# Kernel tuning notes

Measured on AMD Instinct MI355X. Metric: run time of the kernel, lower is better.

Reference implementation:

```python
import jax, jax.numpy as jnp
import numpy as np

HEADS = 8
DIM_HEAD = 32  # dim // heads


def setup_inputs() -> dict:
    key = jax.random.key(0)
    ks = jax.random.split(key, 5)
    B, C, H, W = 4, 256, 48, 48
    return {
        "x": jax.random.normal(ks[0], (B, C, H, W), jnp.float32),
        "Wqkv": jax.random.normal(ks[1], (3 * C, C), jnp.float32) * (C ** -0.5),
        "bqkv": jax.random.normal(ks[2], (3 * C,), jnp.float32) * 0.02,
        "W0": jax.random.normal(ks[3], (C, C), jnp.float32) * (C ** -0.5),
        "b0": jax.random.normal(ks[4], (C,), jnp.float32) * 0.02,
    }


def reference(x, Wqkv, bqkv, W0, b0):
    b, c, h, w = x.shape
    m, d = HEADS, DIM_HEAD
    n = h * w
    scale = d ** -0.5
    # 1x1 conv == per-pixel GEMM: [b,3c,h,w]
    qkv = jnp.einsum('bchw,oc->bohw', x, Wqkv) + bqkv[None, :, None, None]
    # rearrange 'b (d k m) h w -> k b m (h w) d' (channel factors as d, then k, then m)
    qkv = qkv.reshape(b, d, 3, m, n)            # [b, d, 3, m, n]
    qkv = jnp.transpose(qkv, (2, 0, 3, 4, 1))   # [3, b, m, n, d]
    q, k, v = qkv[0], qkv[1], qkv[2]
    scores = jnp.einsum('bmid,bmjd->bmij', q, k) * scale  # [b, m, n, n]
    attn = jax.nn.softmax(scores, axis=-1)
    out = jnp.einsum('bmij,bmjd->bmid', attn, v)          # [b, m, n, d]
    # rearrange 'b m (h w) d -> b (m d) h w'
    out = jnp.transpose(out, (0, 1, 3, 2)).reshape(b, m * d, h, w)
    out = jnp.einsum('bchw,oc->bohw', out, W0) + b0[None, :, None, None]
    return out
```

## Files before the change

kernel.cpp:

```cpp
#include <hip/hip_runtime.h>
#include <hip/hip_bf16.h>

#define NPIX 2304
#define C_IN 256
#define NHEADS 8
#define DHEAD 32

typedef float f32x4 __attribute__((ext_vector_type(4)));
typedef __bf16 bf16x8 __attribute__((ext_vector_type(8)));
typedef __bf16 bf16x4 __attribute__((ext_vector_type(4)));

#if __has_builtin(__builtin_amdgcn_exp2f)
#define EXP2F(x) __builtin_amdgcn_exp2f(x)
#else
#define EXP2F(x) exp2f(x)
#endif

__device__ inline void gload_lds16(const void* g, void* l) {
    __builtin_amdgcn_global_load_lds(
        (const __attribute__((address_space(1))) unsigned int*)g,
        (__attribute__((address_space(3))) unsigned int*)l, 16, 0, 0);
}

__global__ __launch_bounds__(256) void prep_w(
    const float* __restrict__ Wq, const float* __restrict__ W0,
    __bf16* __restrict__ wq, __bf16* __restrict__ w0)
{
    const int r = blockIdx.x;
    const int c = threadIdx.x;
    float v;
    __bf16* dst;
    if (r < 768) { v = Wq[r * 256 + c];         dst = wq + (size_t)r * 512; }
    else         { v = W0[(r - 768) * 256 + c]; dst = w0 + (size_t)(r - 768) * 512; }
    __bf16 hb = (__bf16)v;
    dst[c]       = hb;
    dst[256 + c] = (__bf16)(v - (float)hb);
}

__global__ __launch_bounds__(256) void prep_x(
    const float* __restrict__ x, __bf16* __restrict__ xt)
{
    __shared__ unsigned int lds[64 * 69];
    const int t  = threadIdx.x;
    const int n0 = blockIdx.x * 64;
    const int c0 = blockIdx.y * 64;
    const int b  = blockIdx.z;
    const float* xb = x + (size_t)b * C_IN * NPIX;

    #pragma unroll
    for (int p = 0; p < 4; ++p) {
        const int r    = (t >> 4) + p * 16;
        const int ncol = (t & 15) * 4;
        float4 v = *(const float4*)&xb[(size_t)(c0 + r) * NPIX + n0 + ncol];
        float a[4] = {v.x, v.y, v.z, v.w};
        #pragma unroll
        for (int i = 0; i < 4; ++i)
            lds[r * 69 + ncol + i] =
                (unsigned int)__builtin_bit_cast(unsigned short, (__bf16)a[i]);
    }
    __syncthreads();

    #pragma unroll
    for (int p = 0; p < 2; ++p) {
        const int nn = (t >> 3) + p * 32;
        const int ch = t & 7;
        bf16x8 h8;
        #pragma unroll
        for (int i = 0; i < 8; ++i)
            h8[i] = __builtin_bit_cast(__bf16,
                        (unsigned short)lds[(ch * 8 + i) * 69 + nn]);
        *(bf16x8*)&xt[((size_t)b * NPIX + n0 + nn) * 256 + c0 + ch * 8] = h8;
    }
}

__global__ __launch_bounds__(256) void qkv_mfma(
    const __bf16* __restrict__ wq, const __bf16* __restrict__ xt,
    const float* __restrict__ bias, float* __restrict__ qg,
    __bf16* __restrict__ khi, __bf16* __restrict__ vg)
{
    __shared__ alignas(16) unsigned char sm[32768];
    const int tid = threadIdx.x;
    const int l   = tid & 63;
    const int w   = tid >> 6;
    const int g   = l >> 4;
    const int c16 = l & 15;

    const int id  = blockIdx.x;
    const int xcd = id & 7;
    const int li  = id >> 3;
    const int pnl = xcd * 9 + li / 6;
    const int mt  = li % 6;
    const int b   = pnl / 18;
    const int nt  = pnl - b * 18;
    const int n0  = nt * 128;
    const int p0  = mt * 128;
    const int kq  = mt >> 1;

    const int wr = (w >> 1) * 64;
    const int wc = (w & 1) * 64;
    f32x4 acc[4][4] = {};

#define STG(buf, ks)                                                           \
    {                                                                          \
        unsigned char* lbs = sm + (buf) * 16384;                               \
        _Pragma("unroll")                                                      \
        for (int i = 0; i < 2; ++i) {                                          \
            const int row = i * 64 + (tid >> 2);                               \
            const int cl  = tid & 3;                                           \
            const int cg  = cl ^ (row & 3);                                    \
            const int pA  = p0 + row;                                          \
            const int oA  = 24 * ((pA & 255) >> 3) + 8 * kq + (pA & 7);        \
            gload_lds16(wq + (size_t)oA * 512 + (ks) * 32 + cg * 8,            \
                        lbs + row * 64 + cl * 16);                             \
            gload_lds16(xt + ((size_t)b * NPIX + n0 + row) * 256 +             \
                            ((ks) & 7) * 32 + cg * 8,                          \
                        lbs + 8192 + row * 64 + cl * 16);                      \
        }                                                                      \
    }

    STG(0, 0);
    __syncthreads();
    for (int ks = 0; ks < 16; ++ks) {
        const int buf = ks & 1;
        if (ks + 1 < 16) STG(buf ^ 1, ks + 1);
        unsigned char* lb = sm + buf * 16384;
        bf16x8 af[4], bff[4];
        #pragma unroll
        for (int oi = 0; oi < 4; ++oi) {
            const int ra = wr + oi * 16 + c16;
            af[oi] = *(bf16x8*)(lb + ra * 64 + ((g ^ (ra & 3)) * 16));
        }
        #pragma unroll
        for (int ni = 0; ni < 4; ++ni) {
            const int rb = wc + ni * 16 + c16;
            bff[ni] = *(bf16x8*)(lb + 8192 + rb * 64 + ((g ^ (rb & 3)) * 16));
        }
        #pragma unroll
        for (int oi = 0; oi < 4; ++oi)
            #pragma unroll
            for (int ni = 0; ni < 4; ++ni)
                acc[oi][ni] = __builtin_amdgcn_mfma_f32_16x16x32_bf16(
                    af[oi], bff[ni], acc[oi][ni], 0, 0, 0);
        __syncthreads();
    }
#undef STG

    const float qscale = 0.17677669529663687f * 1.4426950408889634f;
    #pragma unroll
    for (int oi = 0; oi < 4; ++oi) {
        #pragma unroll
        for (int rr = 0; rr < 4; ++rr) {
            const int p = p0 + wr + oi * 16 + 4 * g + rr;
            const int d = (p & 255) >> 3;
            const int h = p & 7;
            const int o = 24 * d + 8 * kq + h;
            const float bi = bias[o];
            const int bh_ = b * NHEADS + h;
            #pragma unroll
            for (int ni = 0; ni < 4; ++ni) {
                const int n = n0 + wc + ni * 16 + c16;
                const float val = acc[oi][ni][rr] + bi;
                if (kq == 0) {
                    qg[((size_t)bh_ * DHEAD + d) * NPIX + n] = val * qscale;
                } else if (kq == 1) {
                    const int cp = ((d >> 3) + (n >> 1)) & 3;
                    khi[((size_t)bh_ * NPIX + n) * 32 + cp * 8 + (d & 7)] = (__bf16)val;
                } else {
                    const int cp = ((n >> 3) & 7) ^ (d & 7);
                    vg[((size_t)bh_ * DHEAD + d) * NPIX + (n >> 6) * 64 + cp * 8 + (n & 7)]
                        = (__bf16)val;
                }
            }
        }
    }
}

__global__ __launch_bounds__(256) void attn_mfma(
    const float* __restrict__ qg, const __bf16* __restrict__ khi,
    const __bf16* __restrict__ vg,
    float* __restrict__ po, float* __restrict__ lw)
{
    __shared__ alignas(16) unsigned char sm[32768];
    const int tid = threadIdx.x;
    const int l   = tid & 63;
    const int w   = tid >> 6;
    const int g   = l >> 4;
    const int c16 = l & 15;

    const int id = blockIdx.x;
    const int lg = (id & 7) * 144 + (id >> 3);
    const int bh = lg / 36;
    const int rem = lg - bh * 36;
    const int half = rem / 18;
    const int qt = rem - half * 18;

    const float*  qb  = qg  + (size_t)bh * DHEAD * NPIX;
    const __bf16* khb = khi + (size_t)bh * NPIX * 32;
    const __bf16* vb  = vg  + (size_t)bh * DHEAD * NPIX;

    const int q0 = qt * 128 + w * 32;

    bf16x8 qh[2], ql[2];
    #pragma unroll
    for (int qgi = 0; qgi < 2; ++qgi)
        #pragma unroll
        for (int e = 0; e < 8; ++e) {
            float v = qb[(size_t)(g * 8 + e) * NPIX + q0 + qgi * 16 + c16];
            __bf16 hb = (__bf16)v;
            qh[qgi][e] = hb;
            ql[qgi][e] = (__bf16)(v - (float)hb);
        }

    f32x4 o[2][2] = {};
    float lsum[2] = {0.f, 0.f};

    const int vd   = w * 8 + (l >> 3);
    const int kswz = (c16 >> 1) & 3;
    unsigned char* const wsl = sm + 16384 + w * 4096;

#define STAGE(buf, kb)                                                         \
    {                                                                          \
        const int j0s = (kb) * 64;                                             \
        unsigned char* lbs = sm + (buf) * 8192;                                \
        gload_lds16(khb + (size_t)(j0s + w * 16) * 32 + l * 8, lbs + w * 1024);\
        gload_lds16(vb + (size_t)vd * NPIX + j0s + (l & 7) * 8,                \
                    lbs + 4096 + w * 1024);                                    \
    }

    const int kb0 = half * 18;
    STAGE(0, kb0);
    __syncthreads();

    for (int t = 0; t < 18; ++t) {
        const int buf = t & 1;
        if (t + 1 < 18) STAGE(buf ^ 1, kb0 + t + 1);
        unsigned char* lb = sm + buf * 8192;

        f32x4 sv[2][4];
        __builtin_amdgcn_s_setprio(1);
        #pragma unroll
        for (int f = 0; f < 4; ++f) {
            const int ko = (c16 + 16 * f) * 64 + ((g + kswz) & 3) * 16;
            bf16x8 kh8 = *(bf16x8*)(lb + ko);
            #pragma unroll
            for (int qgi = 0; qgi < 2; ++qgi) {
                f32x4 acc = {0.f, 0.f, 0.f, 0.f};
                acc = __builtin_amdgcn_mfma_f32_16x16x32_bf16(kh8, ql[qgi], acc, 0, 0, 0);
                acc = __builtin_amdgcn_mfma_f32_16x16x32_bf16(kh8, qh[qgi], acc, 0, 0, 0);
                sv[qgi][f] = acc;
            }
        }
        __builtin_amdgcn_s_setprio(0);

        #pragma unroll
        for (int qgi = 0; qgi < 2; ++qgi) {
            float rs = 0.f;
            __bf16 pb[16];
            #pragma unroll
            for (int f = 0; f < 4; ++f)
                #pragma unroll
                for (int rr = 0; rr < 4; ++rr) {
                    const float p = EXP2F(sv[qgi][f][rr]);
                    rs += p;
                    pb[f * 4 + rr] = (__bf16)p;
                }
            lsum[qgi] += rs;
            const int qrow = qgi * 16 + c16;
            #pragma unroll
            for (int f = 0; f < 4; ++f) {
                const int ch = (2 * f + (g >> 1)) ^ (c16 & 7);
                *(bf16x4*)(wsl + qrow * 128 + ch * 16 + (g & 1) * 8) =
                    *(bf16x4*)&pb[f * 4];
            }
        }

        __builtin_amdgcn_s_setprio(1);
        #pragma unroll
        for (int kc = 0; kc < 2; ++kc) {
            const int vch = (((g + 4 * kc) ^ (c16 & 7))) * 16;
            bf16x8 va0 = *(bf16x8*)(lb + 4096 + c16 * 128 + vch);
            bf16x8 va1 = *(bf16x8*)(lb + 4096 + (16 + c16) * 128 + vch);
            #pragma unroll
            for (int qgi = 0; qgi < 2; ++qgi) {
                bf16x8 pf = *(bf16x8*)(wsl + (qgi * 16 + c16) * 128 + vch);
                o[qgi][0] = __builtin_amdgcn_mfma_f32_16x16x32_bf16(va0, pf, o[qgi][0], 0, 0, 0);
                o[qgi][1] = __builtin_amdgcn_mfma_f32_16x16x32_bf16(va1, pf, o[qgi][1], 0, 0, 0);
            }
        }
        __builtin_amdgcn_s_setprio(0);

        __syncthreads();
    }
#undef STAGE

    #pragma unroll
    for (int qgi = 0; qgi < 2; ++qgi) {
        lsum[qgi] += __shfl_xor(lsum[qgi], 16);
        lsum[qgi] += __shfl_xor(lsum[qgi], 32);
        const int n = q0 + qgi * 16 + c16;
        const size_t rbase = ((size_t)(half * 32 + bh) * NPIX + n) * 32;
        #pragma unroll
        for (int dh = 0; dh < 2; ++dh)
            *(f32x4*)&po[rbase + dh * 16 + 4 * g] = o[qgi][dh];
        if (g == 0)
            lw[(size_t)(half * 32 + bh) * NPIX + n] = lsum[qgi];
    }
}

__global__ __launch_bounds__(256) void combine(
    const float* __restrict__ po, const float* __restrict__ lw,
    __bf16* __restrict__ aw)
{
    const int t  = threadIdx.x;
    const int nn = t >> 6;
    const int r  = t & 63;
    const int h  = r >> 3;
    const int d4 = (r & 7) * 4;
    const int n0 = blockIdx.x * 16;
    const int b  = blockIdx.y;
    const int bh = b * NHEADS + h;

    #pragma unroll
    for (int p = 0; p < 4; ++p) {
        const int n = n0 + p * 4 + nn;
        const float inv = 1.0f / (lw[(size_t)bh * NPIX + n] +
                                  lw[(size_t)(32 + bh) * NPIX + n]);
        f32x4 O0 = *(const f32x4*)&po[((size_t)bh * NPIX + n) * 32 + d4];
        f32x4 O1 = *(const f32x4*)&po[((size_t)(32 + bh) * NPIX + n) * 32 + d4];
        bf16x4 hv;
        #pragma unroll
        for (int i = 0; i < 4; ++i)
            hv[i] = (__bf16)((O0[i] + O1[i]) * inv);
        *(bf16x4*)&aw[((size_t)b * NPIX + n) * 256 + h * 32 + d4] = hv;
    }
}

__global__ __launch_bounds__(256) void out_mfma(
    const __bf16* __restrict__ w0, const __bf16* __restrict__ aw,
    const float* __restrict__ bias, float* __restrict__ out)
{
    __shared__ alignas(16) unsigned char sm[32768];
    const int tid = threadIdx.x;
    const int l   = tid & 63;
    const int w   = tid >> 6;
    const int g   = l >> 4;
    const int c16 = l & 15;

    const int id  = blockIdx.x;
    const int xcd = id & 7;
    const int li  = id >> 3;
    const int pnl = xcd * 9 + (li >> 1);
    const int mt  = li & 1;
    const int b   = pnl / 18;
    const int nt  = pnl - b * 18;
    const int n0  = nt * 128;
    const int o0  = mt * 128;

    const int wr = (w >> 1) * 64;
    const int wc = (w & 1) * 64;
    f32x4 acc[4][4] = {};

#define STG(buf, ks)                                                           \
    {                                                                          \
        unsigned char* lbs = sm + (buf) * 16384;                               \
        _Pragma("unroll")                                                      \
        for (int i = 0; i < 2; ++i) {                                          \
            const int row = i * 64 + (tid >> 2);                               \
            const int cl  = tid & 3;                                           \
            const int cg  = cl ^ (row & 3);                                    \
            gload_lds16(w0 + (size_t)(o0 + row) * 512 + (ks) * 32 + cg * 8,    \
                        lbs + row * 64 + cl * 16);                             \
            gload_lds16(aw + ((size_t)b * NPIX + n0 + row) * 256 +             \
                            ((ks) & 7) * 32 + cg * 8,                          \
                        lbs + 8192 + row * 64 + cl * 16);                      \
        }                                                                      \
    }

    STG(0, 0);
    __syncthreads();
    for (int ks = 0; ks < 16; ++ks) {
        const int buf = ks & 1;
        if (ks + 1 < 16) STG(buf ^ 1, ks + 1);
        unsigned char* lb = sm + buf * 16384;
        bf16x8 af[4], bff[4];
        #pragma unroll
        for (int oi = 0; oi < 4; ++oi) {
            const int ra = wr + oi * 16 + c16;
            af[oi] = *(bf16x8*)(lb + ra * 64 + ((g ^ (ra & 3)) * 16));
        }
        #pragma unroll
        for (int ni = 0; ni < 4; ++ni) {
            const int rb = wc + ni * 16 + c16;
            bff[ni] = *(bf16x8*)(lb + 8192 + rb * 64 + ((g ^ (rb & 3)) * 16));
        }
        #pragma unroll
        for (int oi = 0; oi < 4; ++oi)
            #pragma unroll
            for (int ni = 0; ni < 4; ++ni)
                acc[oi][ni] = __builtin_amdgcn_mfma_f32_16x16x32_bf16(
                    af[oi], bff[ni], acc[oi][ni], 0, 0, 0);
        __syncthreads();
    }
#undef STG

    #pragma unroll
    for (int oi = 0; oi < 4; ++oi) {
        #pragma unroll
        for (int rr = 0; rr < 4; ++rr) {
            const int o = o0 + wr + oi * 16 + 4 * g + rr;
            const float bi = bias[o];
            #pragma unroll
            for (int ni = 0; ni < 4; ++ni) {
                const int n = n0 + wc + ni * 16 + c16;
                out[((size_t)b * C_IN + o) * NPIX + n] = acc[oi][ni][rr] + bi;
            }
        }
    }
}

extern "C" void kernel_launch(void* const* d_in, const int* in_sizes, int n_in,
                              void* d_out, int out_size, void* d_ws, size_t ws_size,
                              hipStream_t stream) {
    const float* x    = (const float*)d_in[0];
    const float* Wqkv = (const float*)d_in[1];
    const float* bqkv = (const float*)d_in[2];
    const float* W0   = (const float*)d_in[3];
    const float* b0   = (const float*)d_in[4];
    float* out = (float*)d_out;

    char* ws = (char*)d_ws;
    __bf16* wq  = (__bf16*)(ws);
    __bf16* w0  = (__bf16*)(ws + 786432);
    __bf16* xt  = (__bf16*)(ws + 1048576);
    float*  qg  = (float*) (ws + 5767168);
    __bf16* khi = (__bf16*)(ws + 15204352);
    __bf16* vg  = (__bf16*)(ws + 19922944);
    float*  po  = (float*) (ws + 24641536);
    float*  lw  = (float*) (ws + 43515904);
    __bf16* aw  = xt;

    prep_w<<<1024, 256, 0, stream>>>(Wqkv, W0, wq, w0);
    prep_x<<<dim3(NPIX / 64, C_IN / 64, 4), 256, 0, stream>>>(x, xt);
    qkv_mfma<<<dim3(432), 256, 0, stream>>>(wq, xt, bqkv, qg, khi, vg);
    attn_mfma<<<dim3(1152), 256, 0, stream>>>(qg, khi, vg, po, lw);
    combine<<<dim3(NPIX / 16, 4), 256, 0, stream>>>(po, lw, aw);
    out_mfma<<<dim3(144), 256, 0, stream>>>(w0, aw, b0, out);
}
```

Baseline: 159.2 us.

## Fuse prep kernels, fold combine into output GEMM, restructure split-bf16 K loop

Measured after the change: 156.8 us. Within noise of the previous version (-1.5%).

```diff
diff --git a/kernel.cpp b/kernel.cpp
--- a/kernel.cpp
+++ b/kernel.cpp
@@ -22,29 +22,31 @@
         (__attribute__((address_space(3))) unsigned int*)l, 16, 0, 0);
 }
 
-__global__ __launch_bounds__(256) void prep_w(
+__global__ __launch_bounds__(256) void prep_wx(
     const float* __restrict__ Wq, const float* __restrict__ W0,
-    __bf16* __restrict__ wq, __bf16* __restrict__ w0)
-{
-    const int r = blockIdx.x;
-    const int c = threadIdx.x;
-    float v;
-    __bf16* dst;
-    if (r < 768) { v = Wq[r * 256 + c];         dst = wq + (size_t)r * 512; }
-    else         { v = W0[(r - 768) * 256 + c]; dst = w0 + (size_t)(r - 768) * 512; }
-    __bf16 hb = (__bf16)v;
-    dst[c]       = hb;
-    dst[256 + c] = (__bf16)(v - (float)hb);
-}
-
-__global__ __launch_bounds__(256) void prep_x(
-    const float* __restrict__ x, __bf16* __restrict__ xt)
+    const float* __restrict__ x,
+    __bf16* __restrict__ wq, __bf16* __restrict__ w0,
+    __bf16* __restrict__ xt)
 {
     __shared__ unsigned int lds[64 * 69];
+    const int id = blockIdx.x;
     const int t  = threadIdx.x;
-    const int n0 = blockIdx.x * 64;
-    const int c0 = blockIdx.y * 64;
-    const int b  = blockIdx.z;
+
+    if (id >= 576) {
+        const int r = id - 576;
+        float v;
+        __bf16* dst;
+        if (r < 768) { v = Wq[r * 256 + t];         dst = wq + (size_t)r * 512; }
+        else         { v = W0[(r - 768) * 256 + t]; dst = w0 + (size_t)(r - 768) * 512; }
+        __bf16 hb = (__bf16)v;
+        dst[t]       = hb;
+        dst[256 + t] = (__bf16)(v - (float)hb);
+        return;
+    }
+
+    const int n0 = (id % 36) * 64;
+    const int c0 = ((id / 36) & 3) * 64;
+    const int b  = id / 144;
     const float* xb = x + (size_t)b * C_IN * NPIX;
 
     #pragma unroll
@@ -78,7 +80,7 @@
     const float* __restrict__ bias, float* __restrict__ qg,
     __bf16* __restrict__ khi, __bf16* __restrict__ vg)
 {
-    __shared__ alignas(16) unsigned char sm[32768];
+    __shared__ alignas(16) unsigned char sm[49152];
     const int tid = threadIdx.x;
     const int l   = tid & 63;
     const int w   = tid >> 6;
@@ -100,47 +102,59 @@
     const int wc = (w & 1) * 64;
     f32x4 acc[4][4] = {};
 
-#define STG(buf, ks)                                                           \
+#define STG(buf, cs)                                                           \
     {                                                                          \
-        unsigned char* lbs = sm + (buf) * 16384;                               \
+        unsigned char* lbs = sm + (buf) * 24576;                               \
+        _Pragma("unroll")                                                      \
+        for (int i = 0; i < 4; ++i) {                                          \
+            const int row = i * 64 + (tid >> 2);                               \
+            const int cl  = tid & 3;                                           \
+            const int cg  = cl ^ (row & 3);                                    \
+            const int pr  = p0 + (row & 127);                                  \
+            const int oA  = 24 * ((pr & 255) >> 3) + 8 * kq + (pr & 7);        \
+            gload_lds16(wq + (size_t)oA * 512 + (i >> 1) * 256 +               \
+                            (cs) * 32 + cg * 8,                                \
+                        lbs + row * 64 + cl * 16);                             \
+        }                                                                      \
         _Pragma("unroll")                                                      \
         for (int i = 0; i < 2; ++i) {                                          \
             const int row = i * 64 + (tid >> 2);                               \
             const int cl  = tid & 3;                                           \
             const int cg  = cl ^ (row & 3);                                    \
-            const int pA  = p0 + row;                                          \
-            const int oA  = 24 * ((pA & 255) >> 3) + 8 * kq + (pA & 7);        \
-            gload_lds16(wq + (size_t)oA * 512 + (ks) * 32 + cg * 8,            \
-                        lbs + row * 64 + cl * 16);                             \
             gload_lds16(xt + ((size_t)b * NPIX + n0 + row) * 256 +             \
-                            ((ks) & 7) * 32 + cg * 8,                          \
-                        lbs + 8192 + row * 64 + cl * 16);                      \
+                            (cs) * 32 + cg * 8,                                \
+                        lbs + 16384 + row * 64 + cl * 16);                     \
         }                                                                      \
     }
 
     STG(0, 0);
     __syncthreads();
-    for (int ks = 0; ks < 16; ++ks) {
-        const int buf = ks & 1;
-        if (ks + 1 < 16) STG(buf ^ 1, ks + 1);
-        unsigned char* lb = sm + buf * 16384;
-        bf16x8 af[4], bff[4];
+    #pragma unroll
+    for (int cs = 0; cs < 8; ++cs) {
+        const int buf = cs & 1;
+        if (cs + 1 < 8) STG(buf ^ 1, cs + 1);
+        unsigned char* lb = sm + buf * 24576;
+        bf16x8 ah[4], al4[4], bf4[4];
         #pragma unroll
         for (int oi = 0; oi < 4; ++oi) {
             const int ra = wr + oi * 16 + c16;
-            af[oi] = *(bf16x8*)(lb + ra * 64 + ((g ^ (ra & 3)) * 16));
+            ah[oi]  = *(bf16x8*)(lb + ra * 64 + ((g ^ (ra & 3)) * 16));
+            al4[oi] = *(bf16x8*)(lb + (128 + ra) * 64 + ((g ^ (ra & 3)) * 16));
         }
         #pragma unroll
         for (int ni = 0; ni < 4; ++ni) {
             const int rb = wc + ni * 16 + c16;
-            bff[ni] = *(bf16x8*)(lb + 8192 + rb * 64 + ((g ^ (rb & 3)) * 16));
+            bf4[ni] = *(bf16x8*)(lb + 16384 + rb * 64 + ((g ^ (rb & 3)) * 16));
         }
         #pragma unroll
         for (int oi = 0; oi < 4; ++oi)
             #pragma unroll
-            for (int ni = 0; ni < 4; ++ni)
+            for (int ni = 0; ni < 4; ++ni) {
                 acc[oi][ni] = __builtin_amdgcn_mfma_f32_16x16x32_bf16(
-                    af[oi], bff[ni], acc[oi][ni], 0, 0, 0);
+                    ah[oi], bf4[ni], acc[oi][ni], 0, 0, 0);
+                acc[oi][ni] = __builtin_amdgcn_mfma_f32_16x16x32_bf16(
+                    al4[oi], bf4[ni], acc[oi][ni], 0, 0, 0);
+            }
         __syncthreads();
     }
 #undef STG
@@ -307,39 +321,12 @@
     }
 }
 
-__global__ __launch_bounds__(256) void combine(
-    const float* __restrict__ po, const float* __restrict__ lw,
-    __bf16* __restrict__ aw)
+__global__ __launch_bounds__(256) void out_mfma(
+    const __bf16* __restrict__ w0, const float* __restrict__ po,
+    const float* __restrict__ lw, const float* __restrict__ bias,
+    float* __restrict__ out)
 {
-    const int t  = threadIdx.x;
-    const int nn = t >> 6;
-    const int r  = t & 63;
-    const int h  = r >> 3;
-    const int d4 = (r & 7) * 4;
-    const int n0 = blockIdx.x * 16;
-    const int b  = blockIdx.y;
-    const int bh = b * NHEADS + h;
-
-    #pragma unroll
-    for (int p = 0; p < 4; ++p) {
-        const int n = n0 + p * 4 + nn;
-        const float inv = 1.0f / (lw[(size_t)bh * NPIX + n] +
-                                  lw[(size_t)(32 + bh) * NPIX + n]);
-        f32x4 O0 = *(const f32x4*)&po[((size_t)bh * NPIX + n) * 32 + d4];
-        f32x4 O1 = *(const f32x4*)&po[((size_t)(32 + bh) * NPIX + n) * 32 + d4];
-        bf16x4 hv;
-        #pragma unroll
-        for (int i = 0; i < 4; ++i)
-            hv[i] = (__bf16)((O0[i] + O1[i]) * inv);
-        *(bf16x4*)&aw[((size_t)b * NPIX + n) * 256 + h * 32 + d4] = hv;
-    }
-}
-
-__global__ __launch_bounds__(256) void out_mfma(
-    const __bf16* __restrict__ w0, const __bf16* __restrict__ aw,
-    const float* __restrict__ bias, float* __restrict__ out)
-{
-    __shared__ alignas(16) unsigned char sm[32768];
+    __shared__ alignas(16) unsigned char sm[51200];
     const int tid = threadIdx.x;
     const int l   = tid & 63;
     const int w   = tid >> 6;
@@ -360,48 +347,97 @@
     const int wc = (w & 1) * 64;
     f32x4 acc[4][4] = {};
 
-#define STG(buf, ks)                                                           \
+    const int brow = tid >> 1;
+    const int bch  = tid & 1;
+
+#define STG_A(buf, cs)                                                         \
     {                                                                          \
-        unsigned char* lbs = sm + (buf) * 16384;                               \
+        unsigned char* lbs = sm + (buf) * 25600;                               \
         _Pragma("unroll")                                                      \
-        for (int i = 0; i < 2; ++i) {                                          \
+        for (int i = 0; i < 4; ++i) {                                          \
             const int row = i * 64 + (tid >> 2);                               \
             const int cl  = tid & 3;                                           \
             const int cg  = cl ^ (row & 3);                                    \
-            gload_lds16(w0 + (size_t)(o0 + row) * 512 + (ks) * 32 + cg * 8,    \
+            gload_lds16(w0 + (size_t)(o0 + (row & 127)) * 512 +                \
+                            (i >> 1) * 256 + (cs) * 32 + cg * 8,               \
                         lbs + row * 64 + cl * 16);                             \
-            gload_lds16(aw + ((size_t)b * NPIX + n0 + row) * 256 +             \
-                            ((ks) & 7) * 32 + cg * 8,                          \
-                        lbs + 8192 + row * 64 + cl * 16);                      \
         }                                                                      \
     }
 
-    STG(0, 0);
+    f32x4 r0[4], r1[4];
+    float il;
+
+#define LDB(cs)                                                                \
+    {                                                                          \
+        const int bh_ = b * 8 + (cs);                                          \
+        const int n   = n0 + brow;                                             \
+        const float l0 = lw[(size_t)bh_ * NPIX + n];                           \
+        const float l1 = lw[(size_t)(32 + bh_) * NPIX + n];                    \
+        il = 1.0f / (l0 + l1);                                                 \
+        const float* s0 = &po[((size_t)bh_ * NPIX + n) * 32 + bch * 16];       \
+        const float* s1 = &po[((size_t)(32 + bh_) * NPIX + n) * 32 + bch * 16];\
+        _Pragma("unroll")                                                      \
+        for (int k2 = 0; k2 < 4; ++k2) {                                       \
+            r0[k2] = *(const f32x4*)(s0 + k2 * 4);                             \
+            r1[k2] = *(const f32x4*)(s1 + k2 * 4);                             \
+        }                                                                      \
+    }
+
+#define WRB(buf)                                                               \
+    {                                                                          \
+        unsigned char* lbs = sm + (buf) * 25600 + 16384;                       \
+        _Pragma("unroll")                                                      \
+        for (int k2 = 0; k2 < 2; ++k2) {                                       \
+            bf16x8 v8;                                                         \
+            _Pragma("unroll")                                                  \
+            for (int e = 0; e < 4; ++e) {                                      \
+                v8[e]     = (__bf16)((r0[2 * k2][e]     + r1[2 * k2][e])     * il); \
+                v8[4 + e] = (__bf16)((r0[2 * k2 + 1][e] + r1[2 * k2 + 1][e]) * il); \
+            }                                                                  \
+            *(bf16x8*)(lbs + brow * 72 + bch * 32 + k2 * 16) = v8;             \
+        }                                                                      \
+    }
+
+    STG_A(0, 0);
+    LDB(0);
+    WRB(0);
     __syncthreads();
-    for (int ks = 0; ks < 16; ++ks) {
-        const int buf = ks & 1;
-        if (ks + 1 < 16) STG(buf ^ 1, ks + 1);
-        unsigned char* lb = sm + buf * 16384;
-        bf16x8 af[4], bff[4];
+
+    #pragma unroll
+    for (int cs = 0; cs < 8; ++cs) {
+        const int buf = cs & 1;
+        if (cs + 1 < 8) {
+            STG_A(buf ^ 1, cs + 1);
+            LDB(cs + 1);
+        }
+        unsigned char* lb = sm + buf * 25600;
+        bf16x8 ah[4], al4[4], bf4[4];
         #pragma unroll
         for (int oi = 0; oi < 4; ++oi) {
             const int ra = wr + oi * 16 + c16;
-            af[oi] = *(bf16x8*)(lb + ra * 64 + ((g ^ (ra & 3)) * 16));
+            ah[oi]  = *(bf16x8*)(lb + ra * 64 + ((g ^ (ra & 3)) * 16));
+            al4[oi] = *(bf16x8*)(lb + (128 + ra) * 64 + ((g ^ (ra & 3)) * 16));
         }
         #pragma unroll
         for (int ni = 0; ni < 4; ++ni) {
             const int rb = wc + ni * 16 + c16;
-            bff[ni] = *(bf16x8*)(lb + 8192 + rb * 64 + ((g ^ (rb & 3)) * 16));
+            bf4[ni] = *(bf16x8*)(lb + 16384 + rb * 72 + g * 16);
         }
         #pragma unroll
         for (int oi = 0; oi < 4; ++oi)
             #pragma unroll
-            for (int ni = 0; ni < 4; ++ni)
+            for (int ni = 0; ni < 4; ++ni) {
                 acc[oi][ni] = __builtin_amdgcn_mfma_f32_16x16x32_bf16(
-                    af[oi], bff[ni], acc[oi][ni], 0, 0, 0);
+                    ah[oi], bf4[ni], acc[oi][ni], 0, 0, 0);
+                acc[oi][ni] = __builtin_amdgcn_mfma_f32_16x16x32_bf16(
+                    al4[oi], bf4[ni], acc[oi][ni], 0, 0, 0);
+            }
+        if (cs + 1 < 8) WRB(buf ^ 1);
         __syncthreads();
     }
-#undef STG
+#undef STG_A
+#undef LDB
+#undef WRB
 
     #pragma unroll
     for (int oi = 0; oi < 4; ++oi) {
@@ -437,12 +473,9 @@
     __bf16* vg  = (__bf16*)(ws + 19922944);
     float*  po  = (float*) (ws + 24641536);
     float*  lw  = (float*) (ws + 43515904);
-    __bf16* aw  = xt;
-
-    prep_w<<<1024, 256, 0, stream>>>(Wqkv, W0, wq, w0);
-    prep_x<<<dim3(NPIX / 64, C_IN / 64, 4), 256, 0, stream>>>(x, xt);
+
+    prep_wx<<<dim3(1600), 256, 0, stream>>>(Wqkv, W0, x, wq, w0, xt);
     qkv_mfma<<<dim3(432), 256, 0, stream>>>(wq, xt, bqkv, qg, khi, vg);
     attn_mfma<<<dim3(1152), 256, 0, stream>>>(qg, khi, vg, po, lw);
-    combine<<<dim3(NPIX / 16, 4), 256, 0, stream>>>(po, lw, aw);
-    out_mfma<<<dim3(144), 256, 0, stream>>>(w0, aw, b0, out);
-}
+    out_mfma<<<dim3(144), 256, 0, stream>>>(w0, po, lw, b0, out);
+}
```
